# Kernel optimization log

Hardware: AMD Instinct MI355X
Metric: run time of the kernel (lower is better)

## Reference

```python
import jax, jax.numpy as jnp
import numpy as np

N, C = 1048576, 128
GAMMA = 2.0
SMOOTHING = 0.1


def setup_inputs() -> dict:
    key = jax.random.key(0)
    k1, k2, k3, k4, k5 = jax.random.split(key, 5)
    inputs = jax.random.normal(k1, (N, C), dtype=jnp.float32)
    targets = jax.random.randint(k2, (N,), 0, C)
    class_weights = jax.random.uniform(k3, (C,), minval=0.5, maxval=2.0, dtype=jnp.float32)
    hot = (jax.random.uniform(k4, (C, C)) > 0.9).astype(jnp.float32)
    extra = jax.random.uniform(k5, (C, C), minval=0.0, maxval=2.0, dtype=jnp.float32)
    penalty_matrix = 1.0 + hot * extra
    penalty_matrix = penalty_matrix * (1.0 - jnp.eye(C, dtype=jnp.float32)) + jnp.eye(C, dtype=jnp.float32)
    return {"inputs": inputs, "targets": targets,
            "class_weights": class_weights, "penalty_matrix": penalty_matrix}


def reference(inputs, targets, class_weights, penalty_matrix):
    num_classes = inputs.shape[-1]
    # label smoothing on one-hot targets
    one_hot = jax.nn.one_hot(targets, num_classes, dtype=inputs.dtype)  # [N, C]
    smooth_targets = one_hot * (1.0 - SMOOTHING) + SMOOTHING / num_classes
    log_probs = jax.nn.log_softmax(inputs, axis=-1)  # [N, C]
    probs = jnp.exp(log_probs)
    focal_weights = (1.0 - probs) ** GAMMA
    base_loss = -(focal_weights * smooth_targets * log_probs).sum(axis=-1)  # [N]
    base_loss = base_loss * class_weights[targets]
    # confusion penalty: sum_{j != t} max(P[t, j] - 1, 0) * probs[:, j]
    # (original loop only adds when p > 1.0 and skips j == i)
    excess = jnp.maximum(penalty_matrix - 1.0, 0.0)
    excess = excess * (1.0 - jnp.eye(num_classes, dtype=inputs.dtype))
    confusion_penalty = (excess[targets] * probs).sum(axis=-1)  # [N]
    return (base_loss + confusion_penalty).mean()
```

## Files before the change

### kernel.cpp

```cpp
#include <hip/hip_runtime.h>


#define NROWS 1048576
#define NCLS  128
#define BLOCK 256
#define GRID  4096

#define WPB    (BLOCK / 64)
#define NWAVES (GRID * WPB)
#define NQUADS (NROWS / 4)
#define QPW    (NQUADS / NWAVES)

constexpr float SMOOTH_OFF = 0.1f / 128.0f;
constexpr float SMOOTH_ON  = 0.9f;

using f4 = __attribute__((ext_vector_type(4))) float;

template <int CTRL>
__device__ __forceinline__ float row_rot(float v) {
    int r = __builtin_amdgcn_update_dpp(__float_as_int(v), __float_as_int(v),
                                        CTRL, 0xF, 0xF, false);
    return __int_as_float(r);
}
__device__ __forceinline__ float grpmax16(float v) {
    v = fmaxf(v, row_rot<0x128>(v));
    v = fmaxf(v, row_rot<0x124>(v));
    v = fmaxf(v, row_rot<0x122>(v));
    v = fmaxf(v, row_rot<0x121>(v));
    return v;
}
__device__ __forceinline__ float grpsum16(float v) {
    v += row_rot<0x128>(v);
    v += row_rot<0x124>(v);
    v += row_rot<0x122>(v);
    v += row_rot<0x121>(v);
    return v;
}

template <bool PRE>
__device__ __forceinline__ float do_slot(
    f4& A, f4& B, int& t, int qpre,
    const f4* __restrict__ in4, const int* __restrict__ targets,
    const float* __restrict__ cls_w, const float* __restrict__ P,
    int lane, int g, int q16, int jb)
{
    const float cw = cls_w[t];
    const f4* prow = reinterpret_cast<const f4*>(P + (size_t)t * NCLS);
    const f4 pa = prow[2 * q16];
    const f4 pb = prow[2 * q16 + 1];

    const f4  Ac = A;
    const f4  Bc = B;
    const int tc = t;

    if (PRE) {
        A = __builtin_nontemporal_load(in4 + (size_t)qpre * 128 + lane * 2);
        B = __builtin_nontemporal_load(in4 + (size_t)qpre * 128 + lane * 2 + 1);
        t = targets[qpre * 4 + g];
    }

    float m = fmaxf(fmaxf(fmaxf(Ac[0], Ac[1]), fmaxf(Ac[2], Ac[3])),
                    fmaxf(fmaxf(Bc[0], Bc[1]), fmaxf(Bc[2], Bc[3])));
    m = grpmax16(m);

    float ev[8];
    #pragma unroll
    for (int k = 0; k < 4; ++k) ev[k]     = __expf(Ac[k] - m);
    #pragma unroll
    for (int k = 0; k < 4; ++k) ev[4 + k] = __expf(Bc[k] - m);

    float z = ((ev[0] + ev[1]) + (ev[2] + ev[3]))
            + ((ev[4] + ev[5]) + (ev[6] + ev[7]));
    z = grpsum16(z);

    const float mlz = m + __logf(z);
    const float rZ  = 1.0f / z;

    float s1 = 0.0f, te = 0.0f, pen = 0.0f;
    #pragma unroll
    for (int k = 0; k < 8; ++k) {
        const float x   = (k < 4) ? Ac[k] : Bc[k - 4];
        const float pvk = (k < 4) ? pa[k] : pb[k - 4];
        const float lp  = x - mlz;
        const float p   = ev[k] * rZ;
        const float om  = 1.0f - p;
        const float fl  = om * om * lp;
        s1  += fl;
        if (jb + k == tc) te = fl;
        pen += fmaxf(pvk - 1.0f, 0.0f) * p;
    }
    return pen - cw * (SMOOTH_OFF * s1 + SMOOTH_ON * te);
}

__global__ __launch_bounds__(BLOCK) void focal_main(
    const float* __restrict__ inputs,
    const int*   __restrict__ targets,
    const float* __restrict__ cls_w,
    const float* __restrict__ P,
    float*       __restrict__ partial)
{
    const int tid  = threadIdx.x;
    const int lane = tid & 63;
    const int wib  = tid >> 6;
    const int g    = lane >> 4;
    const int q16  = lane & 15;
    const int jb   = q16 * 8;

    const int waveId = blockIdx.x * WPB + wib;
    const f4* in4 = reinterpret_cast<const f4*>(inputs);

    const int qb = waveId * QPW;

    f4 A0 = __builtin_nontemporal_load(in4 + (size_t)(qb + 0) * 128 + lane * 2);
    f4 B0 = __builtin_nontemporal_load(in4 + (size_t)(qb + 0) * 128 + lane * 2 + 1);
    f4 A1 = __builtin_nontemporal_load(in4 + (size_t)(qb + 1) * 128 + lane * 2);
    f4 B1 = __builtin_nontemporal_load(in4 + (size_t)(qb + 1) * 128 + lane * 2 + 1);
    f4 A2 = __builtin_nontemporal_load(in4 + (size_t)(qb + 2) * 128 + lane * 2);
    f4 B2 = __builtin_nontemporal_load(in4 + (size_t)(qb + 2) * 128 + lane * 2 + 1);
    f4 A3 = __builtin_nontemporal_load(in4 + (size_t)(qb + 3) * 128 + lane * 2);
    f4 B3 = __builtin_nontemporal_load(in4 + (size_t)(qb + 3) * 128 + lane * 2 + 1);
    int t0 = targets[(qb + 0) * 4 + g];
    int t1 = targets[(qb + 1) * 4 + g];
    int t2 = targets[(qb + 2) * 4 + g];
    int t3 = targets[(qb + 3) * 4 + g];

    float acc = 0.0f;

    for (int it = 0; it < QPW - 4; it += 4) {
        acc += do_slot<true>(A0, B0, t0, qb + it + 4, in4, targets, cls_w, P, lane, g, q16, jb);
        acc += do_slot<true>(A1, B1, t1, qb + it + 5, in4, targets, cls_w, P, lane, g, q16, jb);
        acc += do_slot<true>(A2, B2, t2, qb + it + 6, in4, targets, cls_w, P, lane, g, q16, jb);
        acc += do_slot<true>(A3, B3, t3, qb + it + 7, in4, targets, cls_w, P, lane, g, q16, jb);
    }
    acc += do_slot<false>(A0, B0, t0, 0, in4, targets, cls_w, P, lane, g, q16, jb);
    acc += do_slot<false>(A1, B1, t1, 0, in4, targets, cls_w, P, lane, g, q16, jb);
    acc += do_slot<false>(A2, B2, t2, 0, in4, targets, cls_w, P, lane, g, q16, jb);
    acc += do_slot<false>(A3, B3, t3, 0, in4, targets, cls_w, P, lane, g, q16, jb);

    #pragma unroll
    for (int off = 32; off > 0; off >>= 1)
        acc += __shfl_xor(acc, off, 64);

    __shared__ float ssum[WPB];
    if (lane == 0) ssum[wib] = acc;
    __syncthreads();
    if (tid == 0) {
        float s = 0.0f;
        #pragma unroll
        for (int w = 0; w < WPB; ++w) s += ssum[w];
        partial[blockIdx.x] = s;
    }
}

__global__ __launch_bounds__(256) void focal_final(
    const float* __restrict__ partial, float* __restrict__ out)
{
    double s = 0.0;
    for (int i = threadIdx.x; i < GRID; i += 256) s += (double)partial[i];

    #pragma unroll
    for (int off = 32; off > 0; off >>= 1)
        s += __shfl_xor(s, off, 64);

    __shared__ double sh[4];
    const int wave = threadIdx.x >> 6;
    if ((threadIdx.x & 63) == 0) sh[wave] = s;
    __syncthreads();
    if (threadIdx.x == 0) {
        double tot = sh[0] + sh[1] + sh[2] + sh[3];
        out[0] = (float)(tot / (double)NROWS);
    }
}

extern "C" void kernel_launch(void* const* d_in, const int* in_sizes, int n_in,
                              void* d_out, int out_size, void* d_ws, size_t ws_size,
                              hipStream_t stream) {
    const float* inputs  = (const float*)d_in[0];
    const int*   targets = (const int*)  d_in[1];
    const float* cls_w   = (const float*)d_in[2];
    const float* P       = (const float*)d_in[3];
    float* out     = (float*)d_out;
    float* partial = (float*)d_ws;

    focal_main<<<GRID, BLOCK, 0, stream>>>(inputs, targets, cls_w, P, partial);
    focal_final<<<1, 256, 0, stream>>>(partial, out);
}
```

Measured before the change: 702.8 us.

## Use single-stage prefetch with halved grid and higher occupancy bound

Replaces the four-deep register prefetch ring with a one-row-ahead prefetch, halves the grid so each wave handles twice as many row quads, and adds a min-blocks launch bound of 8. The aim is to cut register pressure so more waves fit per CU and let occupancy hide memory latency instead of deep per-wave buffering. The risk is less in-flight memory per wave, so total outstanding loads may drop if occupancy does not rise enough.

```diff
diff --git a/kernel.cpp b/kernel.cpp
--- a/kernel.cpp
+++ b/kernel.cpp
@@ -4,7 +4,7 @@
 #define NROWS 1048576
 #define NCLS  128
 #define BLOCK 256
-#define GRID  4096
+#define GRID  2048
 
 #define WPB    (BLOCK / 64)
 #define NWAVES (GRID * WPB)
@@ -37,28 +37,10 @@
     return v;
 }
 
-template <bool PRE>
-__device__ __forceinline__ float do_slot(
-    f4& A, f4& B, int& t, int qpre,
-    const f4* __restrict__ in4, const int* __restrict__ targets,
-    const float* __restrict__ cls_w, const float* __restrict__ P,
-    int lane, int g, int q16, int jb)
+__device__ __forceinline__ float slot_compute(
+    const f4 Ac, const f4 Bc, const int tc,
+    const f4 pa, const f4 pb, const float cw, const int jb)
 {
-    const float cw = cls_w[t];
-    const f4* prow = reinterpret_cast<const f4*>(P + (size_t)t * NCLS);
-    const f4 pa = prow[2 * q16];
-    const f4 pb = prow[2 * q16 + 1];
-
-    const f4  Ac = A;
-    const f4  Bc = B;
-    const int tc = t;
-
-    if (PRE) {
-        A = __builtin_nontemporal_load(in4 + (size_t)qpre * 128 + lane * 2);
-        B = __builtin_nontemporal_load(in4 + (size_t)qpre * 128 + lane * 2 + 1);
-        t = targets[qpre * 4 + g];
-    }
-
     float m = fmaxf(fmaxf(fmaxf(Ac[0], Ac[1]), fmaxf(Ac[2], Ac[3])),
                     fmaxf(fmaxf(Bc[0], Bc[1]), fmaxf(Bc[2], Bc[3])));
     m = grpmax16(m);
@@ -92,7 +74,7 @@
     return pen - cw * (SMOOTH_OFF * s1 + SMOOTH_ON * te);
 }
 
-__global__ __launch_bounds__(BLOCK) void focal_main(
+__global__ __launch_bounds__(BLOCK, 8) void focal_main(
     const float* __restrict__ inputs,
     const int*   __restrict__ targets,
     const float* __restrict__ cls_w,
@@ -111,31 +93,34 @@
 
     const int qb = waveId * QPW;
 
-    f4 A0 = __builtin_nontemporal_load(in4 + (size_t)(qb + 0) * 128 + lane * 2);
-    f4 B0 = __builtin_nontemporal_load(in4 + (size_t)(qb + 0) * 128 + lane * 2 + 1);
-    f4 A1 = __builtin_nontemporal_load(in4 + (size_t)(qb + 1) * 128 + lane * 2);
-    f4 B1 = __builtin_nontemporal_load(in4 + (size_t)(qb + 1) * 128 + lane * 2 + 1);
-    f4 A2 = __builtin_nontemporal_load(in4 + (size_t)(qb + 2) * 128 + lane * 2);
-    f4 B2 = __builtin_nontemporal_load(in4 + (size_t)(qb + 2) * 128 + lane * 2 + 1);
-    f4 A3 = __builtin_nontemporal_load(in4 + (size_t)(qb + 3) * 128 + lane * 2);
-    f4 B3 = __builtin_nontemporal_load(in4 + (size_t)(qb + 3) * 128 + lane * 2 + 1);
-    int t0 = targets[(qb + 0) * 4 + g];
-    int t1 = targets[(qb + 1) * 4 + g];
-    int t2 = targets[(qb + 2) * 4 + g];
-    int t3 = targets[(qb + 3) * 4 + g];
+    f4 A = __builtin_nontemporal_load(in4 + (size_t)qb * 128 + lane * 2);
+    f4 B = __builtin_nontemporal_load(in4 + (size_t)qb * 128 + lane * 2 + 1);
+    int t = targets[qb * 4 + g];
 
     float acc = 0.0f;
 
-    for (int it = 0; it < QPW - 4; it += 4) {
-        acc += do_slot<true>(A0, B0, t0, qb + it + 4, in4, targets, cls_w, P, lane, g, q16, jb);
-        acc += do_slot<true>(A1, B1, t1, qb + it + 5, in4, targets, cls_w, P, lane, g, q16, jb);
-        acc += do_slot<true>(A2, B2, t2, qb + it + 6, in4, targets, cls_w, P, lane, g, q16, jb);
-        acc += do_slot<true>(A3, B3, t3, qb + it + 7, in4, targets, cls_w, P, lane, g, q16, jb);
+    for (int it = 0; it < QPW - 1; ++it) {
+        const float cw = cls_w[t];
+        const f4* prow = reinterpret_cast<const f4*>(P + (size_t)t * NCLS);
+        const f4 pa = prow[2 * q16];
+        const f4 pb = prow[2 * q16 + 1];
+
+        const int qn = qb + it + 1;
+        const f4  An = __builtin_nontemporal_load(in4 + (size_t)qn * 128 + lane * 2);
+        const f4  Bn = __builtin_nontemporal_load(in4 + (size_t)qn * 128 + lane * 2 + 1);
+        const int tn = targets[qn * 4 + g];
+
+        acc += slot_compute(A, B, t, pa, pb, cw, jb);
+
+        A = An; B = Bn; t = tn;
     }
-    acc += do_slot<false>(A0, B0, t0, 0, in4, targets, cls_w, P, lane, g, q16, jb);
-    acc += do_slot<false>(A1, B1, t1, 0, in4, targets, cls_w, P, lane, g, q16, jb);
-    acc += do_slot<false>(A2, B2, t2, 0, in4, targets, cls_w, P, lane, g, q16, jb);
-    acc += do_slot<false>(A3, B3, t3, 0, in4, targets, cls_w, P, lane, g, q16, jb);
+    {
+        const float cw = cls_w[t];
+        const f4* prow = reinterpret_cast<const f4*>(P + (size_t)t * NCLS);
+        const f4 pa = prow[2 * q16];
+        const f4 pb = prow[2 * q16 + 1];
+        acc += slot_compute(A, B, t, pa, pb, cw, jb);
+    }
 
     #pragma unroll
     for (int off = 32; off > 0; off >>= 1)
```

After: 698.9 us. Within noise of the previous version (-0.6%).
